# Kernel tuning notes

Hardware: AMD Instinct MI355X
Metric: run time of the kernel (lower is better)

## Reference

```python
import jax, jax.numpy as jnp
import numpy as np

N = 4096      # nodes
F = 32        # num_features (GATConv in = out per head)
H = 2         # heads
NHID = 64     # per-branch mlp output
C = 10        # num_classes
J = 3         # wavelet filters
E = 65536     # edges (avg degree 16)
G = 13        # num_gat = (3**3 - 1) // 2
NEG_SLOPE = 0.2


def setup_inputs() -> dict:
    key = jax.random.key(0)
    ks = jax.random.split(key, 12)
    sc = np.float32(1.0 / np.sqrt(N))
    g = np.float32(0.1)
    x = jax.random.normal(ks[0], (N, F), jnp.float32)
    edge_index = jax.random.randint(ks[1], (2, E), 0, N)
    U = jax.random.normal(ks[2], (N, N), jnp.float32) * sc
    psi = jax.random.normal(ks[3], (J, N, N), jnp.float32) * sc
    # 13 GATConv(F, F, heads=H) parameter stacks
    gat_W = jax.random.normal(ks[4], (G, F, H * F), jnp.float32) * g
    att_src = jax.random.normal(ks[5], (G, H, F), jnp.float32) * g
    att_dst = jax.random.normal(ks[6], (G, H, F), jnp.float32) * g
    gat_b = jnp.zeros((G, H * F), jnp.float32)
    # 13 branch MLPs: Linear(H*F -> NHID)
    mlp_W = jax.random.normal(ks[7], (G, H * F, NHID), jnp.float32) * g
    mlp_b = jnp.zeros((G, NHID), jnp.float32)
    # final head: Linear(13*NHID -> C)
    out_W = jax.random.normal(ks[8], (G * NHID, C), jnp.float32) * g
    out_b = jnp.zeros((C,), jnp.float32)
    return {"x": x, "edge_index": edge_index, "U": U, "psi": psi,
            "gat_W": gat_W, "att_src": att_src, "att_dst": att_dst,
            "gat_b": gat_b, "mlp_W": mlp_W, "mlp_b": mlp_b,
            "out_W": out_W, "out_b": out_b}


def _gat_branch(coef, W, a_s, a_d, bg, mw, mb, src, dst):
    # GATConv(F, F, heads=H, concat=True) in eval mode, then ELU + Linear.
    h = (coef @ W).reshape(N, H, F)                       # [N,H,F]
    es = jnp.einsum('nhf,hf->nh', h, a_s)                 # src attention logits
    ed = jnp.einsum('nhf,hf->nh', h, a_d)                 # dst attention logits
    e = jax.nn.leaky_relu(es[src] + ed[dst], NEG_SLOPE)   # [E+N,H]
    m = jax.ops.segment_max(e, dst, num_segments=N)       # stable softmax per dst
    w = jnp.exp(e - m[dst])
    z = jax.ops.segment_sum(w, dst, num_segments=N)
    alpha = w / (z[dst] + 1e-16)
    out = jax.ops.segment_sum(alpha[:, :, None] * h[src], dst, num_segments=N)
    out = out.reshape(N, H * F) + bg
    return jax.nn.elu(out) @ mw + mb                      # branch MLP -> [N,NHID]


def reference(x, edge_index, U, psi, gat_W, att_src, att_dst, gat_b,
              mlp_W, mlp_b, out_W, out_b):
    loops = jnp.arange(N)
    src = jnp.concatenate([edge_index[0], loops])         # add_self_loops
    dst = jnp.concatenate([edge_index[1], loops])
    # Scattering tree (layer=3, J=3): 1 + 3 + 9 = 13 coefficient maps.
    af = jnp.abs(x)
    coef0 = U @ af                                        # [N,F]
    y1 = jnp.einsum('jnm,mf->jnf', psi, af)               # level-1 wavelets [J,N,F]
    a1 = jnp.abs(y1)
    coef1 = jnp.einsum('nm,jmf->jnf', U, a1)              # [J,N,F]
    y2 = jnp.einsum('knm,jmf->jknf', psi, a1)             # level-2: psi_k @ |y1_j|
    coef2 = jnp.einsum('nm,jkmf->jknf', U, jnp.abs(y2)).reshape(J * J, N, F)
    coefs = jnp.concatenate([coef0[None], coef1, coef2], axis=0)  # [13,N,F]
    branch = jax.vmap(lambda c, W, a_s, a_d, bg, mw, mb:
                      _gat_branch(c, W, a_s, a_d, bg, mw, mb, src, dst))
    yb = branch(coefs, gat_W, att_src, att_dst, gat_b, mlp_W, mlp_b)  # [13,N,NHID]
    feat = jnp.moveaxis(yb, 0, 1).reshape(N, G * NHID)    # concat branches per node
    logits = jax.nn.elu(feat) @ out_W + out_b             # [N,C]
    return jax.nn.log_softmax(logits, axis=1)
```

## Files before the change

### kernel.cpp

```cpp
#include <hip/hip_runtime.h>
#include <hip/hip_bf16.h>

#define NN 4096
#define FF 32
#define EE 65536
#define GG 13

typedef float floatx4 __attribute__((ext_vector_type(4)));
typedef __bf16 bf16x8 __attribute__((ext_vector_type(8)));
typedef short short8 __attribute__((ext_vector_type(8)));

__device__ inline unsigned short f2bf(float f) {
    unsigned u = __float_as_uint(f);
    u += 0x7FFFu + ((u >> 16) & 1u);
    return (unsigned short)(u >> 16);
}


__global__ void k_prep1(const float* __restrict__ x, unsigned short* __restrict__ B) {
    int tid = blockIdx.x * 256 + threadIdx.x;
    int k = tid >> 5, col = tid & 31;
    float v = fabsf(x[tid]);
    B[(((k >> 5) * 2 + (col >> 4)) << 9) + ((col & 15) << 5) + (k & 31)] = f2bf(v);
}

__global__ void k_prep2(const float* __restrict__ P1, unsigned short* __restrict__ B) {
    int tid = blockIdx.x * 256 + threadIdx.x;
    int k = tid / 96, jf = tid % 96;
    int j = jf >> 5, f = jf & 31;
    float v = fabsf(P1[((1 + j) * NN + k) * FF + f]);
    B[(((k >> 5) * 6 + (jf >> 4)) << 9) + ((jf & 15) << 5) + (k & 31)] = f2bf(v);
}

__global__ void k_prep3(const float* __restrict__ P2, unsigned short* __restrict__ B) {
    int tid = blockIdx.x * 256 + threadIdx.x;
    int k = tid / 288, cc = tid % 288;
    int k3 = cc / 96, jf = cc % 96;
    float v = fabsf(P2[((1 + k3) * NN + k) * 96 + jf]);
    B[(((k >> 5) * 18 + (cc >> 4)) << 9) + ((cc & 15) << 5) + (k & 31)] = f2bf(v);
}

__global__ __launch_bounds__(512) void k_pass1(const float* __restrict__ Umat,
                                               const float* __restrict__ Psi,
                                               const unsigned short* __restrict__ Bfrag,
                                               float* __restrict__ Pout,
                                               unsigned short* __restrict__ Apack) {
    __shared__ float abuf[16 * 516];
    __shared__ float cs[2][16 * 32];
    int tile = blockIdx.x, mat = blockIdx.y;
    const float* A = (mat == 0) ? Umat : (Psi + (size_t)(mat - 1) * NN * NN);
    int tid = threadIdx.x;
    int wave = tid >> 6, lane = tid & 63;
    int c15 = lane & 15, q = lane >> 4;

    const float* atile = A + (size_t)tile * 16 * NN;
    const unsigned short* bbase = Bfrag + (c15 << 5) + (q << 3);
    unsigned short* apk = Apack + ((size_t)mat << 24) + (size_t)tile * 65536
                          + (c15 << 5) + (q << 3);

    floatx4 acc0 = {0.f,0.f,0.f,0.f}, acc1 = {0.f,0.f,0.f,0.f};
    floatx4 v[4];

#pragma unroll
    for (int i = 0; i < 4; i++) {
        int seg = wave * 4 + i, row = seg >> 1, half = seg & 1;
        v[i] = *(const floatx4*)(atile + (size_t)row * NN + half * 256 + lane * 4);
    }
#pragma unroll
    for (int i = 0; i < 4; i++) {
        int seg = wave * 4 + i, row = seg >> 1, half = seg & 1;
        *(floatx4*)(abuf + row * 516 + half * 256 + lane * 4) = v[i];
    }
    __syncthreads();

    for (int chunk = 0; chunk < 8; chunk++) {
        if (chunk < 7) {
#pragma unroll
            for (int i = 0; i < 4; i++) {
                int seg = wave * 4 + i, row = seg >> 1, half = seg & 1;
                v[i] = *(const floatx4*)(atile + (size_t)row * NN + (chunk + 1) * 512
                                         + half * 256 + lane * 4);
            }
        }
#pragma unroll
        for (int t = 0; t < 2; t++) {
            int ksl = wave * 2 + t;
            int ksg = chunk * 16 + ksl;
            short8 bv0 = *(const short8*)(bbase + (size_t)(ksg * 2 + 0) * 512);
            short8 bv1 = *(const short8*)(bbase + (size_t)(ksg * 2 + 1) * 512);
            const float* lp = abuf + c15 * 516 + ksl * 32 + q * 8;
            floatx4 f0 = *(const floatx4*)lp;
            floatx4 f1 = *(const floatx4*)(lp + 4);
            short8 av;
            av[0]=f2bf(f0[0]); av[1]=f2bf(f0[1]); av[2]=f2bf(f0[2]); av[3]=f2bf(f0[3]);
            av[4]=f2bf(f1[0]); av[5]=f2bf(f1[1]); av[6]=f2bf(f1[2]); av[7]=f2bf(f1[3]);
            *(short8*)(apk + (size_t)ksg * 512) = av;
            bf16x8 ab = __builtin_bit_cast(bf16x8, av);
            acc0 = __builtin_amdgcn_mfma_f32_16x16x32_bf16(ab, __builtin_bit_cast(bf16x8, bv0), acc0, 0, 0, 0);
            acc1 = __builtin_amdgcn_mfma_f32_16x16x32_bf16(ab, __builtin_bit_cast(bf16x8, bv1), acc1, 0, 0, 0);
        }
        __syncthreads();
        if (chunk < 7) {
#pragma unroll
            for (int i = 0; i < 4; i++) {
                int seg = wave * 4 + i, row = seg >> 1, half = seg & 1;
                *(floatx4*)(abuf + row * 516 + half * 256 + lane * 4) = v[i];
            }
            __syncthreads();
        }
    }

    int half = wave & 1;
    floatx4 acc[2] = {acc0, acc1};
    for (int w2 = 0; w2 < 4; w2++) {
        if ((wave >> 1) == w2) {
#pragma unroll
            for (int t = 0; t < 2; t++)
#pragma unroll
                for (int r = 0; r < 4; r++) {
                    int idx = (q * 4 + r) * 32 + t * 16 + c15;
                    if (w2 == 0) cs[half][idx] = acc[t][r];
                    else cs[half][idx] += acc[t][r];
                }
        }
        __syncthreads();
    }
    float* orow = Pout + ((size_t)mat * NN + (size_t)tile * 16) * 32;
    for (int i = tid; i < 16 * 32; i += 512) orow[i] = cs[0][i] + cs[1][i];
}

template <int NT, int NTOT>
__global__ __launch_bounds__(512) void k_passP(const unsigned short* __restrict__ Apack,
                                               const unsigned short* __restrict__ Bfrag,
                                               float* __restrict__ Pout) {
    constexpr int NC = NT * 16;
    constexpr int NCTOT = NTOT * 16;
    int tile = blockIdx.x;
    int mat = blockIdx.y;
    int cg = blockIdx.z;
    int tid = threadIdx.x;
    int wave = tid >> 6, lane = tid & 63;
    int c15 = lane & 15, q = lane >> 4;
    const unsigned short* ap = Apack + ((size_t)mat << 24) + (size_t)tile * 65536
                               + (size_t)(wave * 16) * 512 + (c15 << 5) + (q << 3);
    const unsigned short* bbase = Bfrag + (size_t)(wave * 16) * NTOT * 512
                                  + (size_t)(cg * NT) * 512 + (c15 << 5) + (q << 3);

    floatx4 acc[NT];
#pragma unroll
    for (int t = 0; t < NT; t++) acc[t] = (floatx4){0.f, 0.f, 0.f, 0.f};

    short8 af = *(const short8*)ap;
    short8 bv[NT];
#pragma unroll
    for (int t = 0; t < NT; t++) bv[t] = *(const short8*)(bbase + t * 512);

    for (int s = 0; s < 15; s++) {
        short8 af2 = *(const short8*)(ap + (s + 1) * 512);
        short8 bv2[NT];
        const unsigned short* bp = bbase + (size_t)(s + 1) * NTOT * 512;
#pragma unroll
        for (int t = 0; t < NT; t++) bv2[t] = *(const short8*)(bp + t * 512);
        bf16x8 ab = __builtin_bit_cast(bf16x8, af);
#pragma unroll
        for (int t = 0; t < NT; t++)
            acc[t] = __builtin_amdgcn_mfma_f32_16x16x32_bf16(
                ab, __builtin_bit_cast(bf16x8, bv[t]), acc[t], 0, 0, 0);
        af = af2;
#pragma unroll
        for (int t = 0; t < NT; t++) bv[t] = bv2[t];
    }
    {
        bf16x8 ab = __builtin_bit_cast(bf16x8, af);
#pragma unroll
        for (int t = 0; t < NT; t++)
            acc[t] = __builtin_amdgcn_mfma_f32_16x16x32_bf16(
                ab, __builtin_bit_cast(bf16x8, bv[t]), acc[t], 0, 0, 0);
    }

    __shared__ float cs[2][16 * NC];
    int half = wave & 1;
    for (int w2 = 0; w2 < 4; w2++) {
        if ((wave >> 1) == w2) {
#pragma unroll
            for (int t = 0; t < NT; t++)
#pragma unroll
                for (int r = 0; r < 4; r++) {
                    int idx = (q * 4 + r) * NC + t * 16 + c15;
                    if (w2 == 0) cs[half][idx] = acc[t][r];
                    else cs[half][idx] += acc[t][r];
                }
        }
        __syncthreads();
    }
    float* orow = Pout + ((size_t)mat * NN + (size_t)tile * 16) * NCTOT + cg * NC;
    for (int i = tid; i < 16 * NC; i += 512) {
        int r = i / NC, c = i % NC;
        orow[(size_t)r * NCTOT + c] = cs[0][i] + cs[1][i];
    }
}

__global__ void k_hes(const float* __restrict__ P1, const float* __restrict__ P2,
                      const float* __restrict__ P3, const float* __restrict__ gatW,
                      const float* __restrict__ attS, const float* __restrict__ attD,
                      float* __restrict__ h, float* __restrict__ es,
                      float* __restrict__ ed) {
    int w = (blockIdx.x * 256 + threadIdx.x) >> 6;
    int lane = threadIdx.x & 63;
    int g = w >> 12, n = w & 4095;
    const float* crow;
    if (g == 0) crow = P1 + (size_t)n * FF;
    else if (g <= 3) crow = P2 + (size_t)n * 96 + (g - 1) * 32;
    else {
        int j = (g - 4) / 3, k3 = (g - 4) % 3;
        crow = P3 + (size_t)n * 288 + k3 * 96 + j * 32;
    }
    const float* wcol = gatW + g * (32 * 64) + lane;
    float a = 0.f;
#pragma unroll
    for (int f = 0; f < 32; f++) a += crow[f] * wcol[f * 64];
    h[(size_t)w * 64 + lane] = a;
    float vs = a * attS[g * 64 + lane];
    float vd = a * attD[g * 64 + lane];
#pragma unroll
    for (int off = 16; off >= 1; off >>= 1) {
        vs += __shfl_down(vs, off, 32);
        vd += __shfl_down(vd, off, 32);
    }
    if ((lane & 31) == 0) {
        es[w * 2 + (lane >> 5)] = vs;
        ed[w * 2 + (lane >> 5)] = vd;
    }
}

__global__ void k_hist(const int* __restrict__ ei, int* __restrict__ cnt) {
    int e = blockIdx.x * 256 + threadIdx.x;
    int d = (e < EE) ? ei[EE + e] : (e - EE);
    atomicAdd(&cnt[d], 1);
}

__global__ void k_scan(const int* __restrict__ cnt, int* __restrict__ offs,
                       int* __restrict__ cursor) {
    int lane = threadIdx.x;
    int base = lane * 64;
    int s = 0;
    for (int i = 0; i < 64; i++) s += cnt[base + i];
    int x = s;
    for (int d = 1; d < 64; d <<= 1) {
        int y = __shfl_up(x, d);
        if (lane >= d) x += y;
    }
    int run = x - s;
    for (int i = 0; i < 64; i++) {
        offs[base + i] = run;
        cursor[base + i] = run;
        run += cnt[base + i];
    }
}

__global__ void k_scatter(const int* __restrict__ ei, int* __restrict__ cursor,
                          int* __restrict__ csr) {
    int e = blockIdx.x * 256 + threadIdx.x;
    int s, d;
    if (e < EE) { s = ei[e]; d = ei[EE + e]; } else { s = d = e - EE; }
    int pos = atomicAdd(&cursor[d], 1);
    csr[pos] = s;
}

__global__ void k_gat(const float* __restrict__ h, const float* __restrict__ es,
                      const float* __restrict__ ed, const int* __restrict__ offs,
                      const int* __restrict__ cnt, const int* __restrict__ csr,
                      const float* __restrict__ gatb, float* __restrict__ gact) {
    int w = (blockIdx.x * 256 + threadIdx.x) >> 6;
    int lane = threadIdx.x & 63, hh = lane >> 5;
    int g = w >> 12, n = w & 4095;
    float myed = ed[w * 2 + hh];
    float bias = gatb[g * 64 + lane];
    int start = offs[n], deg = cnt[n];
    const float* hg = h + (size_t)g * NN * 64;
    const float* esg = es + (size_t)g * NN * 2;
    int sA = csr[start];
    int sB = (deg > 1) ? csr[start + 1] : 0;
    float hvA = hg[(size_t)sA * 64 + lane];
    float lgA = esg[sA * 2 + hh];
    float m = -INFINITY, z = 0.f, acc = 0.f;
    for (int i = 0; i < deg; i++) {
        int sC = (i + 2 < deg) ? csr[start + i + 2] : 0;
        float hvB = hg[(size_t)sB * 64 + lane];
        float lgB = esg[sB * 2 + hh];
        float lg = lgA + myed;
        lg = (lg > 0.f) ? lg : 0.2f * lg;
        float nm = fmaxf(m, lg);
        float sc = __expf(m - nm);
        float we = __expf(lg - nm);
        z = z * sc + we;
        acc = acc * sc + we * hvA;
        m = nm;
        sA = sB; sB = sC; hvA = hvB; lgA = lgB;
    }
    float o = acc / (z + 1e-16f) + bias;
    o = (o > 0.f) ? o : (__expf(o) - 1.f);
    gact[(size_t)w * 64 + lane] = o;
}

__global__ void k_mlp(const float* __restrict__ gact, const float* __restrict__ mlpW,
                      const float* __restrict__ mlpb, float* __restrict__ feat) {
    int tid = blockIdx.x * 256 + threadIdx.x;
    int g = tid >> 18;
    int n = (tid & ((1 << 18) - 1)) >> 6;
    int k = tid & 63;
    const float* grow = gact + ((size_t)g * NN + n) * 64;
    const float* wc = mlpW + (size_t)g * 64 * 64 + k;
    float a = mlpb[g * 64 + k];
#pragma unroll 8
    for (int i = 0; i < 64; i++) a += grow[i] * wc[i * 64];
    a = (a > 0.f) ? a : (__expf(a) - 1.f);
    feat[(size_t)n * 832 + g * 64 + k] = a;
}

__global__ void k_final(const float* __restrict__ feat, const float* __restrict__ oW,
                        const float* __restrict__ ob, float* __restrict__ out) {
    int w = (blockIdx.x * 256 + threadIdx.x) >> 6;
    int lane = threadIdx.x & 63;
    float a[10];
#pragma unroll
    for (int c = 0; c < 10; c++) a[c] = 0.f;
    const float* frow = feat + (size_t)w * 832;
#pragma unroll
    for (int i = 0; i < 13; i++) {
        float v = frow[i * 64 + lane];
        const float* wp = oW + (i * 64 + lane) * 10;
#pragma unroll
        for (int c = 0; c < 10; c++) a[c] += v * wp[c];
    }
#pragma unroll
    for (int off = 32; off >= 1; off >>= 1)
#pragma unroll
        for (int c = 0; c < 10; c++) a[c] += __shfl_down(a[c], off);
    if (lane == 0) {
        float m = -INFINITY;
#pragma unroll
        for (int c = 0; c < 10; c++) { a[c] += ob[c]; m = fmaxf(m, a[c]); }
        float s = 0.f;
#pragma unroll
        for (int c = 0; c < 10; c++) s += __expf(a[c] - m);
        float lse = m + __logf(s);
#pragma unroll
        for (int c = 0; c < 10; c++) out[w * 10 + c] = a[c] - lse;
    }
}

extern "C" void kernel_launch(void* const* d_in, const int* in_sizes, int n_in,
                              void* d_out, int out_size, void* d_ws, size_t ws_size,
                              hipStream_t stream) {
    const float* x    = (const float*)d_in[0];
    const int*   ei   = (const int*)d_in[1];
    const float* U    = (const float*)d_in[2];
    const float* psi  = (const float*)d_in[3];
    const float* gatW = (const float*)d_in[4];
    const float* attS = (const float*)d_in[5];
    const float* attD = (const float*)d_in[6];
    const float* gatb = (const float*)d_in[7];
    const float* mlpW = (const float*)d_in[8];
    const float* mlpb = (const float*)d_in[9];
    const float* oW   = (const float*)d_in[10];
    const float* ob   = (const float*)d_in[11];
    float* out = (float*)d_out;

    char* ws = (char*)d_ws;
    size_t off = 0;
    auto alloc = [&](size_t bytes) { char* p = ws + off; off += (bytes + 255) & ~(size_t)255; return p; };
    unsigned short* Apack = (unsigned short*)alloc((size_t)4 * NN * NN * 2);
    unsigned short* bf1 = (unsigned short*)alloc((size_t)NN * 32 * 2);
    float* P1           = (float*)alloc((size_t)4 * NN * 32 * 4);
    unsigned short* bf2 = (unsigned short*)alloc((size_t)NN * 96 * 2);
    float* P2           = (float*)alloc((size_t)4 * NN * 96 * 4);
    unsigned short* bf3 = (unsigned short*)alloc((size_t)NN * 288 * 2);
    float* P3           = (float*)alloc((size_t)NN * 288 * 4);
    float* h            = (float*)alloc((size_t)GG * NN * 64 * 4);
    float* es           = (float*)alloc((size_t)GG * NN * 2 * 4);
    float* ed           = (float*)alloc((size_t)GG * NN * 2 * 4);
    int* cnt            = (int*)alloc((size_t)NN * 4);
    int* offs           = (int*)alloc((size_t)NN * 4);
    int* cursor         = (int*)alloc((size_t)NN * 4);
    int* csr            = (int*)alloc((size_t)(EE + NN) * 4);
    float* gact         = (float*)alloc((size_t)GG * NN * 64 * 4);
    float* feat         = (float*)alloc((size_t)NN * 832 * 4);
    (void)ws_size; (void)in_sizes; (void)n_in; (void)out_size;

    hipMemsetAsync(cnt, 0, NN * 4, stream);
    k_hist<<<(EE + NN) / 256, 256, 0, stream>>>(ei, cnt);
    k_scan<<<1, 64, 0, stream>>>(cnt, offs, cursor);
    k_scatter<<<(EE + NN) / 256, 256, 0, stream>>>(ei, cursor, csr);

    k_prep1<<<(NN * 32) / 256, 256, 0, stream>>>(x, bf1);
    k_pass1<<<dim3(NN / 16, 4), 512, 0, stream>>>(U, psi, bf1, P1, Apack);
    k_prep2<<<(NN * 96) / 256, 256, 0, stream>>>(P1, bf2);
    k_passP<6, 6><<<dim3(NN / 16, 4, 1), 512, 0, stream>>>(Apack, bf2, P2);
    k_prep3<<<(NN * 288) / 256, 256, 0, stream>>>(P2, bf3);
    k_passP<6, 18><<<dim3(NN / 16, 1, 3), 512, 0, stream>>>(Apack, bf3, P3);

    k_hes<<<(GG * NN * 64) / 256, 256, 0, stream>>>(P1, P2, P3, gatW, attS, attD, h, es, ed);
    k_gat<<<(GG * NN * 64) / 256, 256, 0, stream>>>(h, es, ed, offs, cnt, csr, gatb, gact);
    k_mlp<<<(GG * NN * 64) / 256, 256, 0, stream>>>(gact, mlpW, mlpb, feat);
    k_final<<<(NN * 64) / 256, 256, 0, stream>>>(feat, oW, ob, out);
}
```

Baseline: 647.7 us.

## Stream A tiles into double-buffered LDS via direct global-to-LDS loads in pass1

```diff
diff --git a/kernel.cpp b/kernel.cpp
--- a/kernel.cpp
+++ b/kernel.cpp
@@ -14,6 +14,12 @@
     unsigned u = __float_as_uint(f);
     u += 0x7FFFu + ((u >> 16) & 1u);
     return (unsigned short)(u >> 16);
+}
+
+__device__ inline void gl2lds16(const float* g, float* l) {
+    __builtin_amdgcn_global_load_lds(
+        (__attribute__((address_space(1))) void*)(void*)(g),
+        (__attribute__((address_space(3))) void*)(l), 16, 0, 0);
 }
 
 
@@ -40,12 +46,12 @@
     B[(((k >> 5) * 18 + (cc >> 4)) << 9) + ((cc & 15) << 5) + (k & 31)] = f2bf(v);
 }
 
-__global__ __launch_bounds__(512) void k_pass1(const float* __restrict__ Umat,
-                                               const float* __restrict__ Psi,
-                                               const unsigned short* __restrict__ Bfrag,
-                                               float* __restrict__ Pout,
-                                               unsigned short* __restrict__ Apack) {
-    __shared__ float abuf[16 * 516];
+__global__ __launch_bounds__(512, 8) void k_pass1(const float* __restrict__ Umat,
+                                                  const float* __restrict__ Psi,
+                                                  const unsigned short* __restrict__ Bfrag,
+                                                  float* __restrict__ Pout,
+                                                  unsigned short* __restrict__ Apack) {
+    __shared__ float abuf[2][16 * 256];
     __shared__ float cs[2][16 * 32];
     int tile = blockIdx.x, mat = blockIdx.y;
     const float* A = (mat == 0) ? Umat : (Psi + (size_t)(mat - 1) * NN * NN);
@@ -58,56 +64,48 @@
     unsigned short* apk = Apack + ((size_t)mat << 24) + (size_t)tile * 65536
                           + (c15 << 5) + (q << 3);
 
-    floatx4 acc0 = {0.f,0.f,0.f,0.f}, acc1 = {0.f,0.f,0.f,0.f};
-    floatx4 v[4];
-
-#pragma unroll
-    for (int i = 0; i < 4; i++) {
-        int seg = wave * 4 + i, row = seg >> 1, half = seg & 1;
-        v[i] = *(const floatx4*)(atile + (size_t)row * NN + half * 256 + lane * 4);
-    }
-#pragma unroll
-    for (int i = 0; i < 4; i++) {
-        int seg = wave * 4 + i, row = seg >> 1, half = seg & 1;
-        *(floatx4*)(abuf + row * 516 + half * 256 + lane * 4) = v[i];
-    }
+    int r0 = 2 * wave, r1 = 2 * wave + 1;
+    const float* g0 = atile + (size_t)r0 * NN + ((lane ^ (r0 & 7)) << 2);
+    const float* g1 = atile + (size_t)r1 * NN + ((lane ^ (r1 & 7)) << 2);
+    float* l0 = &abuf[0][wave * 512];
+    float* l1 = &abuf[1][wave * 512];
+
+    int swz = c15 & 7;
+    int u0 = ((wave * 8 + q * 2 + 0) ^ swz) << 2;
+    int u1 = ((wave * 8 + q * 2 + 1) ^ swz) << 2;
+    int rowbase = c15 << 8;
+
+    floatx4 acc0 = {0.f, 0.f, 0.f, 0.f}, acc1 = {0.f, 0.f, 0.f, 0.f};
+
+    gl2lds16(g0, l0);
+    gl2lds16(g1, l0 + 256);
+    short8 pb0 = *(const short8*)(bbase + (size_t)(wave * 2 + 0) * 512);
+    short8 pb1 = *(const short8*)(bbase + (size_t)(wave * 2 + 1) * 512);
     __syncthreads();
 
-    for (int chunk = 0; chunk < 8; chunk++) {
-        if (chunk < 7) {
-#pragma unroll
-            for (int i = 0; i < 4; i++) {
-                int seg = wave * 4 + i, row = seg >> 1, half = seg & 1;
-                v[i] = *(const floatx4*)(atile + (size_t)row * NN + (chunk + 1) * 512
-                                         + half * 256 + lane * 4);
-            }
+    for (int c = 0; c < 16; c++) {
+        const float* rb = abuf[c & 1];
+        if (c < 15) {
+            float* wbb = (c & 1) ? l0 : l1;
+            gl2lds16(g0 + (size_t)(c + 1) * 256, wbb);
+            gl2lds16(g1 + (size_t)(c + 1) * 256, wbb + 256);
         }
-#pragma unroll
-        for (int t = 0; t < 2; t++) {
-            int ksl = wave * 2 + t;
-            int ksg = chunk * 16 + ksl;
-            short8 bv0 = *(const short8*)(bbase + (size_t)(ksg * 2 + 0) * 512);
-            short8 bv1 = *(const short8*)(bbase + (size_t)(ksg * 2 + 1) * 512);
-            const float* lp = abuf + c15 * 516 + ksl * 32 + q * 8;
-            floatx4 f0 = *(const floatx4*)lp;
-            floatx4 f1 = *(const floatx4*)(lp + 4);
-            short8 av;
-            av[0]=f2bf(f0[0]); av[1]=f2bf(f0[1]); av[2]=f2bf(f0[2]); av[3]=f2bf(f0[3]);
-            av[4]=f2bf(f1[0]); av[5]=f2bf(f1[1]); av[6]=f2bf(f1[2]); av[7]=f2bf(f1[3]);
-            *(short8*)(apk + (size_t)ksg * 512) = av;
-            bf16x8 ab = __builtin_bit_cast(bf16x8, av);
-            acc0 = __builtin_amdgcn_mfma_f32_16x16x32_bf16(ab, __builtin_bit_cast(bf16x8, bv0), acc0, 0, 0, 0);
-            acc1 = __builtin_amdgcn_mfma_f32_16x16x32_bf16(ab, __builtin_bit_cast(bf16x8, bv1), acc1, 0, 0, 0);
+        int ksg = c * 8 + wave;
+        floatx4 f0 = *(const floatx4*)(rb + rowbase + u0);
+        floatx4 f1 = *(const floatx4*)(rb + rowbase + u1);
+        short8 bv0 = pb0, bv1 = pb1;
+        if (c < 15) {
+            pb0 = *(const short8*)(bbase + (size_t)((ksg + 8) * 2 + 0) * 512);
+            pb1 = *(const short8*)(bbase + (size_t)((ksg + 8) * 2 + 1) * 512);
         }
+        short8 av;
+        av[0]=f2bf(f0[0]); av[1]=f2bf(f0[1]); av[2]=f2bf(f0[2]); av[3]=f2bf(f0[3]);
+        av[4]=f2bf(f1[0]); av[5]=f2bf(f1[1]); av[6]=f2bf(f1[2]); av[7]=f2bf(f1[3]);
+        *(short8*)(apk + (size_t)ksg * 512) = av;
+        bf16x8 ab = __builtin_bit_cast(bf16x8, av);
+        acc0 = __builtin_amdgcn_mfma_f32_16x16x32_bf16(ab, __builtin_bit_cast(bf16x8, bv0), acc0, 0, 0, 0);
+        acc1 = __builtin_amdgcn_mfma_f32_16x16x32_bf16(ab, __builtin_bit_cast(bf16x8, bv1), acc1, 0, 0, 0);
         __syncthreads();
-        if (chunk < 7) {
-#pragma unroll
-            for (int i = 0; i < 4; i++) {
-                int seg = wave * 4 + i, row = seg >> 1, half = seg & 1;
-                *(floatx4*)(abuf + row * 516 + half * 256 + lane * 4) = v[i];
-            }
-            __syncthreads();
-        }
     }
 
     int half = wave & 1;
```

After: 651.1 us. Within noise of the previous version (+0.5%).
